# Performance work log

Hardware: AMD Instinct MI355X
Metric: run time of the kernel (lower is better)

## Reference

```python
import jax, jax.numpy as jnp
import numpy as np

DIM, HEADS = 512, 8
HD = DIM // HEADS            # 64
WS = (8, 8)                  # window_size
DS = (2, 2)                  # dilated_size
TW = (WS[0] * DS[0], WS[1] * DS[1])  # total_window_size = (16,16)
SHIFT = (4, 4)


def _rope_tables():
    # Axial 2D RoPE over the (Wh, Ww) window grid: first half of head_dim
    # encodes the h coordinate, second half the w coordinate.
    da = HD // 2
    inv = 1.0 / (10000.0 ** (np.arange(0, da, 2) / da))        # (da/2,)
    ah = np.arange(WS[0])[:, None] * inv                        # (Wh, da/2)
    aw = np.arange(WS[1])[:, None] * inv                        # (Ww, da/2)
    ang = np.concatenate([
        np.broadcast_to(ah[:, None, :], (WS[0], WS[1], da // 2)),
        np.broadcast_to(aw[None, :, :], (WS[0], WS[1], da // 2)),
    ], axis=-1)                                                 # (Wh, Ww, HD/2)
    return jnp.asarray(np.cos(ang), jnp.float32), jnp.asarray(np.sin(ang), jnp.float32)


def _apply_rope(x, cos, sin):
    # x: (M, Wh, Ww, HD); rotate consecutive pairs
    xr = x.reshape(*x.shape[:-1], HD // 2, 2)
    x1, x2 = xr[..., 0], xr[..., 1]
    out = jnp.stack([x1 * cos - x2 * sin, x1 * sin + x2 * cos], axis=-1)
    return out.reshape(x.shape)


def _attn_mask(H, W):
    # Faithful to create_mask (incl. the quirky w_slices where slice(-8,0) is
    # empty and slice(0,None) overwrites the whole row band).
    img = np.zeros((H, W), np.float32)
    cnt = 0
    for hs in (slice(0, -WS[0]), slice(-WS[0], -SHIFT[0]), slice(-SHIFT[0], None)):
        for wsl in (slice(0, -WS[1]), slice(-WS[1], 0), slice(0, None)):
            img[hs, wsl] = cnt
            cnt += 1
    th, tw = TW
    m = img.reshape(H // th, th, W // tw, tw).transpose(0, 2, 1, 3).reshape(-1, th, tw)
    nW = m.shape[0]
    dh, dw = DS
    m = m.reshape(nW, th // dh, dh, tw // dw, dw).transpose(0, 1, 3, 2, 4)
    m = m.reshape(nW, -1, dh * dw).transpose(0, 2, 1).reshape(nW * dh * dw, -1)  # (nW*4, 64)
    diff = m[:, None, :] - m[:, :, None]
    return jnp.asarray(np.where(diff != 0, -1e9, 0.0).astype(np.float32))


def _windows(t):
    # roll -> total-window partition -> dilated partition (Swin-style)
    B, H, W, C = t.shape
    t = jnp.roll(t, (-SHIFT[0], -SHIFT[1]), axis=(1, 2))
    th, tw = TW
    t = t.reshape(B, H // th, th, W // tw, tw, C).transpose(0, 1, 3, 2, 4, 5).reshape(-1, th, tw, C)
    Bw = t.shape[0]                                            # B * nW
    dh, dw = DS
    t = t.reshape(Bw, th // dh, dh, tw // dw, dw, C).transpose(0, 1, 3, 2, 4, 5)
    t = t.reshape(Bw, -1, dh * dw, C).transpose(0, 2, 1, 3).reshape(Bw * dh * dw, -1, C)
    return t, Bw                                               # (Bw*4, 64, C)


def setup_inputs() -> dict:
    key = jax.random.key(0)
    ks = jax.random.split(key, 8)
    B, H, W, C = 4, 128, 128, DIM
    s = 0.02
    return {
        "x": jax.random.normal(ks[0], (B, H, W, C), jnp.float32),
        "cross": jax.random.normal(ks[1], (B, H, W, C), jnp.float32),
        "qv_w": jax.random.normal(ks[2], (C, 2 * C), jnp.float32) * s,
        "qv_b": jnp.zeros((2 * C,), jnp.float32),
        "k_w": jax.random.normal(ks[3], (C, C), jnp.float32) * s,
        "k_b": jnp.zeros((C,), jnp.float32),
        "proj_w": jax.random.normal(ks[4], (C, C), jnp.float32) * s,
        "proj_b": jnp.zeros((C,), jnp.float32),
    }


def reference(x, cross, qv_w, qv_b, k_w, k_b, proj_w, proj_b):
    B, H, W, C = x.shape
    scale = HD ** -0.5
    xw, Bw = _windows(x)
    cw, _ = _windows(cross)
    B_, N, _ = xw.shape                                        # N = 64
    qv = (xw @ qv_w + qv_b).reshape(B_, N, 2, HEADS, HD).transpose(2, 0, 3, 1, 4)
    q, v = qv[0], qv[1]                                        # (B_, h, N, HD)
    k = (cw @ k_w + k_b).reshape(B_, N, HEADS, HD).transpose(0, 2, 1, 3)
    cos, sin = _rope_tables()
    q = _apply_rope(q.reshape(-1, WS[0], WS[1], HD), cos, sin).reshape(B_, HEADS, N, HD)
    k = _apply_rope(k.reshape(-1, WS[0], WS[1], HD), cos, sin).reshape(B_, HEADS, N, HD)
    attn = jnp.einsum('bhnd,bhmd->bhnm', q * scale, k)
    mask = _attn_mask(H, W)                                    # (nW*4, N, N)
    nWd = mask.shape[0]
    attn = attn.reshape(B_ // nWd, nWd, HEADS, N, N) + mask[None, :, None]
    attn = jax.nn.softmax(attn, axis=-1).reshape(B_, HEADS, N, N)
    out = jnp.einsum('bhnm,bhmd->bhnd', attn, v).transpose(0, 2, 1, 3).reshape(B_, N, C)
    # reverse dilation, then reverse total windows, then un-roll
    dh, dw = DS
    th, tw = TW
    out = out.reshape(Bw, dh * dw, N, C).transpose(0, 2, 1, 3).reshape(-1, dh * dw, C)
    out = out.reshape(Bw, th // dh, tw // dw, dh, dw, C).transpose(0, 1, 3, 2, 4, 5).reshape(Bw, th, tw, C)
    out = out.reshape(B, H // th, W // tw, th, tw, C).transpose(0, 1, 3, 2, 4, 5).reshape(B, H, W, C)
    out = jnp.roll(out, (SHIFT[0], SHIFT[1]), axis=(1, 2))
    return out @ proj_w + proj_b
```

## Files before the change

### kernel.cpp

```cpp
#include <hip/hip_runtime.h>


typedef float v4f __attribute__((ext_vector_type(4)));
typedef short short8 __attribute__((ext_vector_type(8)));

#define BM 128
#define BN 128

__device__ __forceinline__ unsigned short f2bf(float f) {
  unsigned int u = __builtin_bit_cast(unsigned int, f);
  u += 0x7fffu + ((u >> 16) & 1u);
  return (unsigned short)(u >> 16);
}

__device__ __forceinline__ int tok2pix(int tok) {
  int g = tok >> 6, n = tok & 63;
  int b = g >> 8, rem = g & 255;
  int d = rem & 3, bw = rem >> 2;
  int wh = bw >> 3, ww = bw & 7;
  int ph = n >> 3, pw = n & 7;
  int ii = (wh * 16 + 2 * ph + (d >> 1) + 4) & 127;
  int jj = (ww * 16 + 2 * pw + (d & 1) + 4) & 127;
  return (b * 128 + ii) * 128 + jj;
}

__global__ __launch_bounds__(256) void prep_kernel(
    const float* __restrict__ qv_w, const float* __restrict__ k_w,
    const float* __restrict__ proj_w,
    unsigned short* __restrict__ qv_wt, unsigned short* __restrict__ k_wt,
    unsigned short* __restrict__ proj_wt,
    float* __restrict__ rope_cos, float* __restrict__ rope_sin) {
  int tid = blockIdx.x * 256 + threadIdx.x;
  if (tid < 524288) {
    int c = tid >> 9, k = tid & 511;
    qv_wt[tid] = f2bf(qv_w[k * 1024 + c]);
  } else if (tid < 786432) {
    int t = tid - 524288;
    int c = t >> 9, k = t & 511;
    k_wt[t] = f2bf(k_w[k * 512 + c]);
  } else if (tid < 1048576) {
    int t = tid - 786432;
    int c = t >> 9, k = t & 511;
    proj_wt[t] = f2bf(proj_w[k * 512 + c]);
  } else if (tid < 1048576 + 2048) {
    int t = tid - 1048576;
    int pos = t >> 5, tt = t & 31;
    int ph = pos >> 3, pw = pos & 7;
    float e = (float)(tt & 15) * (1.0f / 16.0f);
    float inv = powf(10000.0f, -e);
    float ang = (float)(tt < 16 ? ph : pw) * inv;
    rope_cos[t] = cosf(ang);
    rope_sin[t] = sinf(ang);
  }
}

template <int MODE>
__global__ __launch_bounds__(256) void gemm_kernel(
    const void* __restrict__ Ap, const unsigned short* __restrict__ Wt,
    const float* __restrict__ bias, void* __restrict__ out0,
    void* __restrict__ out1, const float* __restrict__ rope_cos,
    const float* __restrict__ rope_sin) {
  __shared__ __attribute__((aligned(16))) unsigned short As[4096];
  __shared__ __attribute__((aligned(16))) unsigned short Bs[4096];
  int tid = threadIdx.x;
  int bm = blockIdx.x, bn = blockIdx.y;
  int lane = tid & 63, wid = tid >> 6;
  int wm = (wid & 1) * 64, wn = (wid >> 1) * 64;
  int l15 = lane & 15, quad = lane >> 4;

  int srow = tid >> 1;
  int shalf = tid & 1;
  int tokA = bm * BM + srow;
  const float* aptr_f = nullptr;
  const unsigned short* aptr_h = nullptr;
  if (MODE == 2) aptr_h = (const unsigned short*)Ap + (size_t)tokA * 512;
  else           aptr_f = (const float*)Ap + (size_t)tok2pix(tokA) * 512;
  const unsigned short* bptr = Wt + (size_t)(bn * BN + srow) * 512;

  v4f acc[4][4];
#pragma unroll
  for (int i = 0; i < 4; i++)
#pragma unroll
    for (int j = 0; j < 4; j++) acc[i][j] = (v4f){0.f, 0.f, 0.f, 0.f};

  for (int k0 = 0; k0 < 512; k0 += 32) {
    if (MODE == 2) {
#pragma unroll
      for (int s = 0; s < 2; s++) {
        int h = shalf * 2 + s;
        short8 v = *(const short8*)(aptr_h + k0 + shalf * 16 + s * 8);
        *(short8*)(As + ((h * 128 + (srow ^ h)) << 3)) = v;
      }
    } else {
#pragma unroll
      for (int s = 0; s < 2; s++) {
        int h = shalf * 2 + s;
        v4f t0 = *(const v4f*)(aptr_f + k0 + shalf * 16 + s * 8);
        v4f t1 = *(const v4f*)(aptr_f + k0 + shalf * 16 + s * 8 + 4);
        short8 w;
        w[0] = (short)f2bf(t0[0]); w[1] = (short)f2bf(t0[1]);
        w[2] = (short)f2bf(t0[2]); w[3] = (short)f2bf(t0[3]);
        w[4] = (short)f2bf(t1[0]); w[5] = (short)f2bf(t1[1]);
        w[6] = (short)f2bf(t1[2]); w[7] = (short)f2bf(t1[3]);
        *(short8*)(As + ((h * 128 + (srow ^ h)) << 3)) = w;
      }
    }
#pragma unroll
    for (int s = 0; s < 2; s++) {
      int h = shalf * 2 + s;
      short8 v = *(const short8*)(bptr + k0 + shalf * 16 + s * 8);
      *(short8*)(Bs + ((h * 128 + (srow ^ h)) << 3)) = v;
    }
    __syncthreads();
    short8 af[4], bfr[4];
#pragma unroll
    for (int i = 0; i < 4; i++)
      af[i] = *(const short8*)(As + ((quad * 128 + ((wm + i * 16 + l15) ^ quad)) << 3));
#pragma unroll
    for (int j = 0; j < 4; j++)
      bfr[j] = *(const short8*)(Bs + ((quad * 128 + ((wn + j * 16 + l15) ^ quad)) << 3));
#pragma unroll
    for (int i = 0; i < 4; i++)
#pragma unroll
      for (int j = 0; j < 4; j++)
        acc[i][j] = __builtin_amdgcn_mfma_f32_16x16x32_bf16(af[i], bfr[j], acc[i][j], 0, 0, 0);
    __syncthreads();
  }

#pragma unroll
  for (int j = 0; j < 4; j++) {
    int col = bn * BN + wn + j * 16 + l15;
    float bv = bias[col];
#pragma unroll
    for (int i = 0; i < 4; i++) {
#pragma unroll
      for (int r = 0; r < 4; r++) {
        int tok = bm * BM + wm + i * 16 + quad * 4 + r;
        float val = acc[i][j][r] + bv;
        if (MODE == 0) {
          int which = col >> 9;
          int h = (col >> 6) & 7;
          int hd = col & 63;
          int g = tok >> 6, n = tok & 63;
          float part = __shfl_xor(val, 1);
          if (which == 0) {
            int ti = (n << 5) + (hd >> 1);
            float c = rope_cos[ti], s = rope_sin[ti];
            float o = (hd & 1) ? (part * s + val * c) : (val * c - part * s);
            o *= 0.125f;
            ((unsigned short*)out0)[(((g * 8 + h) * 64 + n) << 6) + hd] = f2bf(o);
          } else {
            ((unsigned short*)out1)[(((g * 8 + h) * 64 + hd) << 6) + n] = f2bf(val);
          }
        } else if (MODE == 1) {
          int h = (col >> 6) & 7;
          int hd = col & 63;
          int g = tok >> 6, n = tok & 63;
          float part = __shfl_xor(val, 1);
          int ti = (n << 5) + (hd >> 1);
          float c = rope_cos[ti], s = rope_sin[ti];
          float o = (hd & 1) ? (part * s + val * c) : (val * c - part * s);
          ((unsigned short*)out0)[(((g * 8 + h) * 64 + n) << 6) + hd] = f2bf(o);
        } else {
          ((float*)out0)[(size_t)tok2pix(tok) * 512 + col] = val;
        }
      }
    }
  }
}

__global__ __launch_bounds__(256) void attn_kernel(
    const unsigned short* __restrict__ Qbuf, const unsigned short* __restrict__ Kbuf,
    const unsigned short* __restrict__ Vbuf, unsigned short* __restrict__ Obuf) {
  __shared__ __attribute__((aligned(16))) unsigned short Ps[4096];
  int bid = blockIdx.x;
  int g = bid >> 3, h = bid & 7;
  int tid = threadIdx.x;
  int lane = tid & 63, w = tid >> 6;
  int l15 = lane & 15, quad = lane >> 4;
  size_t base = ((size_t)(g * 8 + h)) << 12;
  const unsigned short* Q = Qbuf + base;
  const unsigned short* K = Kbuf + base;
  const unsigned short* Vt = Vbuf + base;

  v4f s[4];
#pragma unroll
  for (int j = 0; j < 4; j++) s[j] = (v4f){0.f, 0.f, 0.f, 0.f};
#pragma unroll
  for (int ki = 0; ki < 2; ki++) {
    short8 aq = *(const short8*)(Q + (w * 16 + l15) * 64 + ki * 32 + quad * 8);
#pragma unroll
    for (int j = 0; j < 4; j++) {
      short8 bk = *(const short8*)(K + (j * 16 + l15) * 64 + ki * 32 + quad * 8);
      s[j] = __builtin_amdgcn_mfma_f32_16x16x32_bf16(aq, bk, s[j], 0, 0, 0);
    }
  }

  int rem = g & 255;
  bool masked_win = ((rem >> 5) == 7);
  float p[4][4];
#pragma unroll
  for (int j = 0; j < 4; j++) {
    int m = j * 16 + l15;
    int pm = m >> 3;
    int gm = (int)(pm >= 4) + (int)(pm >= 6);
#pragma unroll
    for (int r = 0; r < 4; r++) {
      int row = w * 16 + quad * 4 + r;
      int pq = row >> 3;
      int gq = (int)(pq >= 4) + (int)(pq >= 6);
      float v = s[j][r];
      if (masked_win && gm != gq) v = -1e9f;
      p[j][r] = v;
    }
  }
#pragma unroll
  for (int r = 0; r < 4; r++) {
    float mx = fmaxf(fmaxf(p[0][r], p[1][r]), fmaxf(p[2][r], p[3][r]));
    mx = fmaxf(mx, __shfl_xor(mx, 1));
    mx = fmaxf(mx, __shfl_xor(mx, 2));
    mx = fmaxf(mx, __shfl_xor(mx, 4));
    mx = fmaxf(mx, __shfl_xor(mx, 8));
    float sum = 0.f;
#pragma unroll
    for (int j = 0; j < 4; j++) { p[j][r] = __expf(p[j][r] - mx); sum += p[j][r]; }
    sum += __shfl_xor(sum, 1);
    sum += __shfl_xor(sum, 2);
    sum += __shfl_xor(sum, 4);
    sum += __shfl_xor(sum, 8);
    float inv = 1.0f / sum;
    int row = w * 16 + quad * 4 + r;
#pragma unroll
    for (int j = 0; j < 4; j++) {
      int m = j * 16 + l15;
      int h8 = m >> 3;
      Ps[((h8 * 64 + (row ^ h8)) << 3) + (m & 7)] = f2bf(p[j][r] * inv);
    }
  }
  __syncthreads();

  v4f o[4];
#pragma unroll
  for (int j = 0; j < 4; j++) o[j] = (v4f){0.f, 0.f, 0.f, 0.f};
#pragma unroll
  for (int ki = 0; ki < 2; ki++) {
    int h8 = ki * 4 + quad;
    short8 ap = *(const short8*)(Ps + ((h8 * 64 + ((w * 16 + l15) ^ h8)) << 3));
#pragma unroll
    for (int j = 0; j < 4; j++) {
      short8 bv = *(const short8*)(Vt + (j * 16 + l15) * 64 + ki * 32 + quad * 8);
      o[j] = __builtin_amdgcn_mfma_f32_16x16x32_bf16(ap, bv, o[j], 0, 0, 0);
    }
  }
#pragma unroll
  for (int j = 0; j < 4; j++) {
    int hd = j * 16 + l15;
#pragma unroll
    for (int r = 0; r < 4; r++) {
      int row = w * 16 + quad * 4 + r;
      Obuf[(size_t)(g * 64 + row) * 512 + h * 64 + hd] = f2bf(o[j][r]);
    }
  }
}

extern "C" void kernel_launch(void* const* d_in, const int* in_sizes, int n_in,
                              void* d_out, int out_size, void* d_ws, size_t ws_size,
                              hipStream_t stream) {
  const float* x      = (const float*)d_in[0];
  const float* cross  = (const float*)d_in[1];
  const float* qv_w   = (const float*)d_in[2];
  const float* qv_b   = (const float*)d_in[3];
  const float* k_w    = (const float*)d_in[4];
  const float* k_b    = (const float*)d_in[5];
  const float* proj_w = (const float*)d_in[6];
  const float* proj_b = (const float*)d_in[7];

  char* ws = (char*)d_ws;
  const size_t MB = 1024 * 1024;
  unsigned short* Qbuf = (unsigned short*)(ws);
  unsigned short* Kbuf = (unsigned short*)(ws + 64 * MB);
  unsigned short* Vbuf = (unsigned short*)(ws + 128 * MB);
  unsigned short* Obuf = (unsigned short*)(ws + 192 * MB);
  unsigned short* qv_wt = (unsigned short*)(ws + 256 * MB);
  unsigned short* k_wt = qv_wt + 1024 * 512;
  unsigned short* proj_wt = k_wt + 512 * 512;
  float* rope_cos = (float*)(proj_wt + 512 * 512);
  float* rope_sin = rope_cos + 2048;

  prep_kernel<<<4104, 256, 0, stream>>>(qv_w, k_w, proj_w, qv_wt, k_wt, proj_wt,
                                        rope_cos, rope_sin);
  gemm_kernel<0><<<dim3(512, 8), 256, 0, stream>>>(x, qv_wt, qv_b, Qbuf, Vbuf,
                                                   rope_cos, rope_sin);
  gemm_kernel<1><<<dim3(512, 4), 256, 0, stream>>>(cross, k_wt, k_b, Kbuf, nullptr,
                                                   rope_cos, rope_sin);
  attn_kernel<<<8192, 256, 0, stream>>>(Qbuf, Kbuf, Vbuf, Obuf);
  gemm_kernel<2><<<dim3(512, 4), 256, 0, stream>>>(Obuf, proj_wt, proj_b, d_out, nullptr,
                                                   rope_cos, rope_sin);
}
```

Before: 810.3 us.

## Merge QV and K GEMMs, use direct global-to-LDS loads, tile weight transpose

Fuses the QV and K projection GEMMs into one launch, with the column-block index on the fast grid axis so blocks sharing an A tile run close together. B tiles, and in the projection GEMM both operands, now load straight from global memory into LDS with global_load_lds. The A-side fp32-to-bf16 conversion uses packed conversion and a new XOR swizzle. The weight-prep kernel becomes a shared-memory tiled transpose with coalesced reads and writes. The aim is less launch overhead, fewer register round trips and better locality. The risk is LDS bank conflicts in the unswizzled direct-load layout, and the loop still has no double buffering.

New measurement: 817.6 us. No clear change (+0.9%).

```diff
diff --git a/kernel.cpp b/kernel.cpp
--- a/kernel.cpp
+++ b/kernel.cpp
@@ -3,14 +3,30 @@
 
 typedef float v4f __attribute__((ext_vector_type(4)));
 typedef short short8 __attribute__((ext_vector_type(8)));
-
-#define BM 128
-#define BN 128
+typedef unsigned int v4u __attribute__((ext_vector_type(4)));
 
 __device__ __forceinline__ unsigned short f2bf(float f) {
   unsigned int u = __builtin_bit_cast(unsigned int, f);
   u += 0x7fffu + ((u >> 16) & 1u);
   return (unsigned short)(u >> 16);
+}
+
+__device__ __forceinline__ unsigned int pk_bf16(float a, float b) {
+#if __has_builtin(__builtin_amdgcn_cvt_pk_bf16_f32)
+  typedef __bf16 bf2 __attribute__((ext_vector_type(2)));
+  bf2 r = __builtin_amdgcn_cvt_pk_bf16_f32(a, b);
+  return __builtin_bit_cast(unsigned int, r);
+#else
+  return (unsigned int)f2bf(a) | ((unsigned int)f2bf(b) << 16);
+#endif
+}
+
+typedef const __attribute__((address_space(1))) void* gas_t;
+typedef __attribute__((address_space(3))) void* las_t;
+__device__ __forceinline__ void gll16(const void* g, void* l) {
+  __builtin_amdgcn_global_load_lds((gas_t)(unsigned long long)g,
+                                   (las_t)(unsigned int)(unsigned long long)l,
+                                   16, 0, 0);
 }
 
 __device__ __forceinline__ int tok2pix(int tok) {
@@ -30,52 +46,92 @@
     unsigned short* __restrict__ qv_wt, unsigned short* __restrict__ k_wt,
     unsigned short* __restrict__ proj_wt,
     float* __restrict__ rope_cos, float* __restrict__ rope_sin) {
-  int tid = blockIdx.x * 256 + threadIdx.x;
-  if (tid < 524288) {
-    int c = tid >> 9, k = tid & 511;
-    qv_wt[tid] = f2bf(qv_w[k * 1024 + c]);
-  } else if (tid < 786432) {
-    int t = tid - 524288;
-    int c = t >> 9, k = t & 511;
-    k_wt[t] = f2bf(k_w[k * 512 + c]);
-  } else if (tid < 1048576) {
-    int t = tid - 786432;
-    int c = t >> 9, k = t & 511;
-    proj_wt[t] = f2bf(proj_w[k * 512 + c]);
-  } else if (tid < 1048576 + 2048) {
-    int t = tid - 1048576;
-    int pos = t >> 5, tt = t & 31;
-    int ph = pos >> 3, pw = pos & 7;
-    float e = (float)(tt & 15) * (1.0f / 16.0f);
-    float inv = powf(10000.0f, -e);
-    float ang = (float)(tt < 16 ? ph : pw) * inv;
-    rope_cos[t] = cosf(ang);
-    rope_sin[t] = sinf(ang);
-  }
-}
-
-template <int MODE>
-__global__ __launch_bounds__(256) void gemm_kernel(
-    const void* __restrict__ Ap, const unsigned short* __restrict__ Wt,
-    const float* __restrict__ bias, void* __restrict__ out0,
-    void* __restrict__ out1, const float* __restrict__ rope_cos,
-    const float* __restrict__ rope_sin) {
+  int id = blockIdx.x;
+  int t = threadIdx.x;
+  if (id < 256) {
+    __shared__ unsigned short tile[64 * 72];
+    const float* src;
+    unsigned short* dst;
+    int ldin, k0, c0;
+    if (id < 128) {
+      src = qv_w; dst = qv_wt; ldin = 1024;
+      k0 = (id >> 4) * 64; c0 = (id & 15) * 64;
+    } else if (id < 192) {
+      int q = id - 128; src = k_w; dst = k_wt; ldin = 512;
+      k0 = (q >> 3) * 64; c0 = (q & 7) * 64;
+    } else {
+      int q = id - 192; src = proj_w; dst = proj_wt; ldin = 512;
+      k0 = (q >> 3) * 64; c0 = (q & 7) * 64;
+    }
+    int r = t >> 2, cq = t & 3;
+    const float* p = src + (size_t)(k0 + r) * ldin + c0 + cq * 16;
+    v4f f0 = *(const v4f*)(p + 0);
+    v4f f1 = *(const v4f*)(p + 4);
+    v4f f2 = *(const v4f*)(p + 8);
+    v4f f3 = *(const v4f*)(p + 12);
+    unsigned short* tr = tile + r * 72 + cq * 16;
+    tr[0] = f2bf(f0[0]);  tr[1] = f2bf(f0[1]);  tr[2] = f2bf(f0[2]);  tr[3] = f2bf(f0[3]);
+    tr[4] = f2bf(f1[0]);  tr[5] = f2bf(f1[1]);  tr[6] = f2bf(f1[2]);  tr[7] = f2bf(f1[3]);
+    tr[8] = f2bf(f2[0]);  tr[9] = f2bf(f2[1]);  tr[10] = f2bf(f2[2]); tr[11] = f2bf(f2[3]);
+    tr[12] = f2bf(f3[0]); tr[13] = f2bf(f3[1]); tr[14] = f2bf(f3[2]); tr[15] = f2bf(f3[3]);
+    __syncthreads();
+    int cr = t >> 2, kq = t & 3;
+    union { unsigned short s[16]; short8 v[2]; } ob;
+#pragma unroll
+    for (int j = 0; j < 16; j++) ob.s[j] = tile[(kq * 16 + j) * 72 + cr];
+    unsigned short* op = dst + (size_t)(c0 + cr) * 512 + k0 + kq * 16;
+    *(short8*)(op) = ob.v[0];
+    *(short8*)(op + 8) = ob.v[1];
+  } else {
+#pragma unroll
+    for (int e = 0; e < 8; e++) {
+      int idx = t * 8 + e;
+      int pos = idx >> 5, tt = idx & 31;
+      int ph = pos >> 3, pw = pos & 7;
+      float ee = (float)(tt & 15) * (1.0f / 16.0f);
+      float inv = powf(10000.0f, -ee);
+      float ang = (float)(tt < 16 ? ph : pw) * inv;
+      rope_cos[idx] = cosf(ang);
+      rope_sin[idx] = sinf(ang);
+    }
+  }
+}
+
+__global__ __launch_bounds__(256) void gemm_qvk(
+    const float* __restrict__ x, const float* __restrict__ cross,
+    const unsigned short* __restrict__ qv_wt, const unsigned short* __restrict__ k_wt,
+    const float* __restrict__ qv_b, const float* __restrict__ k_b,
+    unsigned short* __restrict__ Qbuf, unsigned short* __restrict__ Kbuf,
+    unsigned short* __restrict__ Vbuf,
+    const float* __restrict__ rope_cos, const float* __restrict__ rope_sin) {
   __shared__ __attribute__((aligned(16))) unsigned short As[4096];
   __shared__ __attribute__((aligned(16))) unsigned short Bs[4096];
-  int tid = threadIdx.x;
-  int bm = blockIdx.x, bn = blockIdx.y;
-  int lane = tid & 63, wid = tid >> 6;
-  int wm = (wid & 1) * 64, wn = (wid >> 1) * 64;
-  int l15 = lane & 15, quad = lane >> 4;
-
-  int srow = tid >> 1;
-  int shalf = tid & 1;
-  int tokA = bm * BM + srow;
-  const float* aptr_f = nullptr;
-  const unsigned short* aptr_h = nullptr;
-  if (MODE == 2) aptr_h = (const unsigned short*)Ap + (size_t)tokA * 512;
-  else           aptr_f = (const float*)Ap + (size_t)tok2pix(tokA) * 512;
-  const unsigned short* bptr = Wt + (size_t)(bn * BN + srow) * 512;
+  const int tid = threadIdx.x;
+  const int bn = blockIdx.x, bm = blockIdx.y;
+  const bool isK = bn >= 8;
+  const float* Asrc = isK ? cross : x;
+  const unsigned short* Wt = isK ? k_wt : qv_wt;
+  const int coln0 = (isK ? bn - 8 : bn) * 128;
+  const int lane = tid & 63, w = tid >> 6;
+  const int l15 = lane & 15, quad = lane >> 4;
+  const int wm = (w & 1) * 64, wn = (w >> 1) * 64;
+  char* AsB = (char*)As;
+  char* BsB = (char*)Bs;
+
+  const int ar = tid >> 1, ah = tid & 1;
+  const float* aptr = Asrc + (size_t)tok2pix(bm * 128 + ar) * 512 + ah * 16;
+  const int au = (ar ^ (ar >> 2)) & 3;
+  const int aoff0 = ar * 64 + (((ah * 2 + 0) ^ au) << 4);
+  const int aoff1 = ar * 64 + (((ah * 2 + 1) ^ au) << 4);
+
+  const unsigned short* bptr[2];
+  int boff[2];
+#pragma unroll
+  for (int s = 0; s < 2; s++) {
+    int rl = w * 32 + s * 16 + (lane >> 2);
+    bptr[s] = Wt + (size_t)(coln0 + rl) * 512 + (lane & 3) * 8;
+    boff[s] = (w * 32 + s * 16) * 64;
+  }
 
   v4f acc[4][4];
 #pragma unroll
@@ -84,41 +140,32 @@
     for (int j = 0; j < 4; j++) acc[i][j] = (v4f){0.f, 0.f, 0.f, 0.f};
 
   for (int k0 = 0; k0 < 512; k0 += 32) {
-    if (MODE == 2) {
-#pragma unroll
-      for (int s = 0; s < 2; s++) {
-        int h = shalf * 2 + s;
-        short8 v = *(const short8*)(aptr_h + k0 + shalf * 16 + s * 8);
-        *(short8*)(As + ((h * 128 + (srow ^ h)) << 3)) = v;
-      }
-    } else {
-#pragma unroll
-      for (int s = 0; s < 2; s++) {
-        int h = shalf * 2 + s;
-        v4f t0 = *(const v4f*)(aptr_f + k0 + shalf * 16 + s * 8);
-        v4f t1 = *(const v4f*)(aptr_f + k0 + shalf * 16 + s * 8 + 4);
-        short8 w;
-        w[0] = (short)f2bf(t0[0]); w[1] = (short)f2bf(t0[1]);
-        w[2] = (short)f2bf(t0[2]); w[3] = (short)f2bf(t0[3]);
-        w[4] = (short)f2bf(t1[0]); w[5] = (short)f2bf(t1[1]);
-        w[6] = (short)f2bf(t1[2]); w[7] = (short)f2bf(t1[3]);
-        *(short8*)(As + ((h * 128 + (srow ^ h)) << 3)) = w;
-      }
-    }
-#pragma unroll
-    for (int s = 0; s < 2; s++) {
-      int h = shalf * 2 + s;
-      short8 v = *(const short8*)(bptr + k0 + shalf * 16 + s * 8);
-      *(short8*)(Bs + ((h * 128 + (srow ^ h)) << 3)) = v;
-    }
+    gll16(bptr[0], BsB + boff[0]);
+    gll16(bptr[1], BsB + boff[1]);
+    bptr[0] += 32;
+    bptr[1] += 32;
+    v4f a0 = *(const v4f*)(aptr + 0);
+    v4f a1 = *(const v4f*)(aptr + 4);
+    v4f a2 = *(const v4f*)(aptr + 8);
+    v4f a3 = *(const v4f*)(aptr + 12);
+    aptr += 32;
+    v4u c0 = (v4u){pk_bf16(a0[0], a0[1]), pk_bf16(a0[2], a0[3]),
+                   pk_bf16(a1[0], a1[1]), pk_bf16(a1[2], a1[3])};
+    v4u c1 = (v4u){pk_bf16(a2[0], a2[1]), pk_bf16(a2[2], a2[3]),
+                   pk_bf16(a3[0], a3[1]), pk_bf16(a3[2], a3[3])};
+    *(v4u*)(AsB + aoff0) = c0;
+    *(v4u*)(AsB + aoff1) = c1;
     __syncthreads();
     short8 af[4], bfr[4];
 #pragma unroll
-    for (int i = 0; i < 4; i++)
-      af[i] = *(const short8*)(As + ((quad * 128 + ((wm + i * 16 + l15) ^ quad)) << 3));
+    for (int i = 0; i < 4; i++) {
+      int r = wm + i * 16 + l15;
+      int u = (r ^ (r >> 2)) & 3;
+      af[i] = *(const short8*)(AsB + r * 64 + ((quad ^ u) << 4));
+    }
 #pragma unroll
     for (int j = 0; j < 4; j++)
-      bfr[j] = *(const short8*)(Bs + ((quad * 128 + ((wn + j * 16 + l15) ^ quad)) << 3));
+      bfr[j] = *(const short8*)(BsB + (wn + j * 16 + l15) * 64 + (quad << 4));
 #pragma unroll
     for (int i = 0; i < 4; i++)
 #pragma unroll
@@ -129,40 +176,29 @@
 
 #pragma unroll
   for (int j = 0; j < 4; j++) {
-    int col = bn * BN + wn + j * 16 + l15;
-    float bv = bias[col];
+    int col = coln0 + wn + j * 16 + l15;
+    float bv = isK ? k_b[col] : qv_b[col];
 #pragma unroll
     for (int i = 0; i < 4; i++) {
 #pragma unroll
       for (int r = 0; r < 4; r++) {
-        int tok = bm * BM + wm + i * 16 + quad * 4 + r;
+        int tok = bm * 128 + wm + i * 16 + quad * 4 + r;
         float val = acc[i][j][r] + bv;
-        if (MODE == 0) {
-          int which = col >> 9;
-          int h = (col >> 6) & 7;
-          int hd = col & 63;
-          int g = tok >> 6, n = tok & 63;
-          float part = __shfl_xor(val, 1);
-          if (which == 0) {
-            int ti = (n << 5) + (hd >> 1);
-            float c = rope_cos[ti], s = rope_sin[ti];
-            float o = (hd & 1) ? (part * s + val * c) : (val * c - part * s);
-            o *= 0.125f;
-            ((unsigned short*)out0)[(((g * 8 + h) * 64 + n) << 6) + hd] = f2bf(o);
-          } else {
-            ((unsigned short*)out1)[(((g * 8 + h) * 64 + hd) << 6) + n] = f2bf(val);
-          }
-        } else if (MODE == 1) {
-          int h = (col >> 6) & 7;
-          int hd = col & 63;
-          int g = tok >> 6, n = tok & 63;
-          float part = __shfl_xor(val, 1);
+        int g = tok >> 6, n = tok & 63;
+        int hh = (col >> 6) & 7, hd = col & 63;
+        float part = __shfl_xor(val, 1);
+        if (!isK && (col >> 9)) {
+          Vbuf[(((g * 8 + hh) * 64 + hd) << 6) + n] = f2bf(val);
+        } else {
           int ti = (n << 5) + (hd >> 1);
           float c = rope_cos[ti], s = rope_sin[ti];
           float o = (hd & 1) ? (part * s + val * c) : (val * c - part * s);
-          ((unsigned short*)out0)[(((g * 8 + h) * 64 + n) << 6) + hd] = f2bf(o);
-        } else {
-          ((float*)out0)[(size_t)tok2pix(tok) * 512 + col] = val;
+          if (!isK) {
+            o *= 0.125f;
+            Qbuf[(((g * 8 + hh) * 64 + n) << 6) + hd] = f2bf(o);
+          } else {
+            Kbuf[(((g * 8 + hh) * 64 + n) << 6) + hd] = f2bf(o);
+          }
         }
       }
     }
@@ -263,6 +299,79 @@
   }
 }
 
+__global__ __launch_bounds__(256) void gemm_proj(
+    const unsigned short* __restrict__ Obuf, const unsigned short* __restrict__ proj_wt,
+    const float* __restrict__ proj_b, float* __restrict__ out) {
+  __shared__ __attribute__((aligned(16))) unsigned short As[4096];
+  __shared__ __attribute__((aligned(16))) unsigned short Bs[4096];
+  const int tid = threadIdx.x;
+  const int bn = blockIdx.x, bm = blockIdx.y;
+  const int coln0 = bn * 128;
+  const int lane = tid & 63, w = tid >> 6;
+  const int l15 = lane & 15, quad = lane >> 4;
+  const int wm = (w & 1) * 64, wn = (w >> 1) * 64;
+  char* AsB = (char*)As;
+  char* BsB = (char*)Bs;
+
+  const unsigned short* aptr[2];
+  const unsigned short* bptr[2];
+  int soff[2];
+#pragma unroll
+  for (int s = 0; s < 2; s++) {
+    int rl = w * 32 + s * 16 + (lane >> 2);
+    aptr[s] = Obuf + (size_t)(bm * 128 + rl) * 512 + (lane & 3) * 8;
+    bptr[s] = proj_wt + (size_t)(coln0 + rl) * 512 + (lane & 3) * 8;
+    soff[s] = (w * 32 + s * 16) * 64;
+  }
+
+  v4f acc[4][4];
+#pragma unroll
+  for (int i = 0; i < 4; i++)
+#pragma unroll
+    for (int j = 0; j < 4; j++) acc[i][j] = (v4f){0.f, 0.f, 0.f, 0.f};
+
+  for (int k0 = 0; k0 < 512; k0 += 32) {
+#pragma unroll
+    for (int s = 0; s < 2; s++) {
+      gll16(aptr[s], AsB + soff[s]);
+      gll16(bptr[s], BsB + soff[s]);
+      aptr[s] += 32;
+      bptr[s] += 32;
+    }
+    __syncthreads();
+    short8 af[4], bfr[4];
+#pragma unroll
+    for (int i = 0; i < 4; i++)
+      af[i] = *(const short8*)(AsB + (wm + i * 16 + l15) * 64 + (quad << 4));
+#pragma unroll
+    for (int j = 0; j < 4; j++)
+      bfr[j] = *(const short8*)(BsB + (wn + j * 16 + l15) * 64 + (quad << 4));
+#pragma unroll
+    for (int i = 0; i < 4; i++)
+#pragma unroll
+      for (int j = 0; j < 4; j++)
+        acc[i][j] = __builtin_amdgcn_mfma_f32_16x16x32_bf16(af[i], bfr[j], acc[i][j], 0, 0, 0);
+    __syncthreads();
+  }
+
+  int pixr[4][4];
+#pragma unroll
+  for (int i = 0; i < 4; i++)
+#pragma unroll
+    for (int r = 0; r < 4; r++)
+      pixr[i][r] = tok2pix(bm * 128 + wm + i * 16 + quad * 4 + r);
+#pragma unroll
+  for (int j = 0; j < 4; j++) {
+    int col = coln0 + wn + j * 16 + l15;
+    float bv = proj_b[col];
+#pragma unroll
+    for (int i = 0; i < 4; i++)
+#pragma unroll
+      for (int r = 0; r < 4; r++)
+        out[(size_t)pixr[i][r] * 512 + col] = acc[i][j][r] + bv;
+  }
+}
+
 extern "C" void kernel_launch(void* const* d_in, const int* in_sizes, int n_in,
                               void* d_out, int out_size, void* d_ws, size_t ws_size,
                               hipStream_t stream) {
@@ -287,13 +396,10 @@
   float* rope_cos = (float*)(proj_wt + 512 * 512);
   float* rope_sin = rope_cos + 2048;
 
-  prep_kernel<<<4104, 256, 0, stream>>>(qv_w, k_w, proj_w, qv_wt, k_wt, proj_wt,
-                                        rope_cos, rope_sin);
-  gemm_kernel<0><<<dim3(512, 8), 256, 0, stream>>>(x, qv_wt, qv_b, Qbuf, Vbuf,
-                                                   rope_cos, rope_sin);
-  gemm_kernel<1><<<dim3(512, 4), 256, 0, stream>>>(cross, k_wt, k_b, Kbuf, nullptr,
-                                                   rope_cos, rope_sin);
+  prep_kernel<<<257, 256, 0, stream>>>(qv_w, k_w, proj_w, qv_wt, k_wt, proj_wt,
+                                       rope_cos, rope_sin);
+  gemm_qvk<<<dim3(12, 512), 256, 0, stream>>>(x, cross, qv_wt, k_wt, qv_b, k_b,
+                                              Qbuf, Kbuf, Vbuf, rope_cos, rope_sin);
   attn_kernel<<<8192, 256, 0, stream>>>(Qbuf, Kbuf, Vbuf, Obuf);
-  gemm_kernel<2><<<dim3(512, 4), 256, 0, stream>>>(Obuf, proj_wt, proj_b, d_out, nullptr,
-                                                   rope_cos, rope_sin);
-}
+  gemm_proj<<<dim3(4, 512), 256, 0, stream>>>(Obuf, proj_wt, proj_b, (float*)d_out);
+}
```
